# Performance work log

Hardware: AMD Instinct MI355X
Metric: run time of the kernel (lower is better)

Reference implementation:

```python
import jax, jax.numpy as jnp
import numpy as np

B, N, D, H = 4, 4096, 1024, 16
DH = D // H          # per-head dim = 64
M = 256              # number of random features
KEPS = 1e-3          # performer kernel epsilon
LNEPS = 1e-5


def setup_inputs() -> dict:
    key = jax.random.key(0)
    ks = jax.random.split(key, 16)
    s = 0.02
    return {
        "src": jax.random.normal(ks[0], (B, N, D), jnp.float32),
        "Wq": s * jax.random.normal(ks[1], (D, D), jnp.float32),
        "Wk": s * jax.random.normal(ks[2], (D, D), jnp.float32),
        "Wv": s * jax.random.normal(ks[3], (D, D), jnp.float32),
        "Wout": s * jax.random.normal(ks[4], (D, D), jnp.float32),
        "b_out": jnp.zeros((D,), jnp.float32),
        "proj": jax.random.normal(ks[5], (M, DH), jnp.float32),
        "g1": jnp.ones((D,), jnp.float32),
        "beta1": jnp.zeros((D,), jnp.float32),
        "W1": s * jax.random.normal(ks[6], (2048, D), jnp.float32),
        "b1": jnp.zeros((2048,), jnp.float32),
        "W2": s * jax.random.normal(ks[7], (D, 2048), jnp.float32),
        "b2": jnp.zeros((D,), jnp.float32),
        "g2": jnp.ones((D,), jnp.float32),
        "beta2": jnp.zeros((D,), jnp.float32),
    }


def _layernorm(x, g, b):
    mu = x.mean(-1, keepdims=True)
    var = ((x - mu) ** 2).mean(-1, keepdims=True)
    return (x - mu) * jax.lax.rsqrt(var + LNEPS) * g + b


def _softmax_kernel(x, proj, is_query):
    # FAVOR+ positive softmax kernel feature map (performer_pytorch)
    dn = DH ** -0.25           # data normalizer d^{-1/4}
    ratio = M ** -0.5
    data_dash = jnp.einsum('bhnd,md->bhnm', x * dn, proj)
    diag = (x ** 2).sum(-1) * 0.5 * dn * dn            # [b,h,n]
    if is_query:
        stab = data_dash.max(-1, keepdims=True)
    else:
        stab = data_dash.max()
    return ratio * (jnp.exp(data_dash - diag[..., None] - stab) + KEPS)


def reference(src, Wq, Wk, Wv, Wout, b_out, proj, g1, beta1, W1, b1, W2, b2, g2, beta2):
    # ---- Performer self-attention (FAVOR+, non-causal) ----
    def split_heads(x):
        return x.reshape(B, N, H, DH).transpose(0, 2, 1, 3)  # [b,h,n,dh]

    q = split_heads(src @ Wq.T)
    k = split_heads(src @ Wk.T)
    v = split_heads(src @ Wv.T)

    qp = _softmax_kernel(q, proj, is_query=True)   # [b,h,n,m]
    kp = _softmax_kernel(k, proj, is_query=False)  # [b,h,n,m]

    k_sum = kp.sum(-2)                                        # [b,h,m]
    d_inv = 1.0 / jnp.einsum('bhnm,bhm->bhn', qp, k_sum)      # [b,h,n]
    context = jnp.einsum('bhnm,bhnd->bhmd', kp, v)            # [b,h,m,dh]
    attn = jnp.einsum('bhnm,bhmd->bhnd', qp, context) * d_inv[..., None]

    attn = attn.transpose(0, 2, 1, 3).reshape(B, N, D)
    src2 = attn @ Wout.T + b_out

    # ---- residual + norm + FFN (dropout = identity at eval) ----
    x = _layernorm(src + src2, g1, beta1)
    ff = (jax.nn.gelu(x @ W1.T + b1, approximate=False)) @ W2.T + b2
    return _layernorm(x + ff, g2, beta2)
```

## Files before the change

kernel.cpp:

```cpp
#include <hip/hip_runtime.h>

#define DEVI __device__ __forceinline__

using u16 = unsigned short;
using u32 = unsigned int;
using u64 = unsigned long long;

typedef __bf16 bf16x8 __attribute__((ext_vector_type(8)));
typedef __bf16 bf16x4 __attribute__((ext_vector_type(4)));
typedef float  f32x4  __attribute__((ext_vector_type(4)));

constexpr int BB = 4, NN = 4096, DD = 1024, HH = 16, DH = 64, MF = 256;
constexpr int RT = BB * NN;
constexpr int QKVS = 3072;
constexpr float DN    = 0.35355339059327373f;
constexpr float RATIO = 0.0625f;
constexpr float DIAGC = 0.0625f;
constexpr float KEPSC = 1e-3f;

DEVI u16 f2bf(float f) {
  u32 u = __float_as_uint(f);
  u32 r = u + 0x7fffu + ((u >> 16) & 1u);
  return (u16)(r >> 16);
}
DEVI float bf2f(u16 u) { return __uint_as_float(((u32)u) << 16); }

typedef void __attribute__((address_space(1)))* gas1;
typedef void __attribute__((address_space(3)))* las3;
DEVI void gload_lds16(const void* g, void* l) {
  __builtin_amdgcn_global_load_lds((gas1)(u64)g, (las3)(u32)(u64)l, 16, 0, 0);
}

DEVI bf16x8 ldswz(const u16* base, int row, int kbyte) {
  int p = (row << 7) + kbyte;
  p ^= (row & 7) << 4;
  return *(const bf16x8*)((const char*)base + p);
}

__global__ void cast_kernel(const float* __restrict__ in, u16* __restrict__ out, int n4) {
  int i = blockIdx.x * 256 + threadIdx.x;
  int stride = gridDim.x * 256;
  for (; i < n4; i += stride) {
    float4 v = ((const float4*)in)[i];
    ushort4 o; o.x = f2bf(v.x); o.y = f2bf(v.y); o.z = f2bf(v.z); o.w = f2bf(v.w);
    ((ushort4*)out)[i] = o;
  }
}

__global__ void cast_weights_kernel(
    const float* __restrict__ Wq, const float* __restrict__ Wk,
    const float* __restrict__ Wv, const float* __restrict__ Wout,
    const float* __restrict__ W1, const float* __restrict__ W2,
    const float* __restrict__ proj,
    u16* __restrict__ wqkvb, u16* __restrict__ wob,
    u16* __restrict__ w1b, u16* __restrict__ w2b, u16* __restrict__ projb)
{
  constexpr int TOT = 2101248;
  int i = blockIdx.x * 256 + threadIdx.x;
  const int stride = gridDim.x * 256;
  for (; i < TOT; i += stride) {
    const float* s; u16* d; int loc; float sc = 1.0f;
    if (i < 1048576) {
      int seg = i >> 18; loc = i & 262143;
      s = (seg == 0) ? Wq : (seg == 1) ? Wk : (seg == 2) ? Wv : Wout;
      d = (seg < 3) ? (wqkvb + seg * 1048576) : wob;
    } else if (i < 1572864) { loc = i - 1048576; s = W1; d = w1b; }
    else if (i < 2097152)   { loc = i - 1572864; s = W2; d = w2b; }
    else                    { loc = i - 2097152; s = proj; d = projb; sc = DN; }
    float4 v = ((const float4*)s)[loc];
    ushort4 o; o.x = f2bf(v.x * sc); o.y = f2bf(v.y * sc); o.z = f2bf(v.z * sc); o.w = f2bf(v.w * sc);
    ((ushort4*)d)[loc] = o;
  }
}

template <int EPI>
__global__ __launch_bounds__(512, 4) void gemm_bt(
    const u16* __restrict__ A, int lda, const u16* __restrict__ Bm,
    u16* __restrict__ Cb, const float* __restrict__ bias,
    int Ncols, int K)
{
  __shared__ __align__(16) u16 sA[256 * 64];
  __shared__ __align__(16) u16 sB[128 * 64];
  const int tid = threadIdx.x, lane = tid & 63;
  const int wv = tid >> 6, wr = wv >> 1, wc = wv & 1;

  const int gx = gridDim.x;
  const int wg = blockIdx.y * gx + blockIdx.x;
  const int cpx = (gx * gridDim.y) >> 3;
  const int swz = (wg & 7) * cpx + (wg >> 3);
  const int bn = swz % gx, bm = swz / gx;

  f32x4 acc[4][4] = {};

  int rowS[4], colS[4], ldsb[4];
#pragma unroll
  for (int it = 0; it < 4; ++it) {
    int p = (it * 512 + tid) * 16;
    ldsb[it] = (it * 512 + (tid & ~63)) * 16;
    int sp = p ^ (((p >> 7) & 7) << 4);
    rowS[it] = sp >> 7;
    colS[it] = (sp >> 1) & 63;
  }
  const size_t baseA = (size_t)bm * 256, baseB = (size_t)bn * 128;

  for (int kt = 0; kt < K; kt += 64) {
#pragma unroll
    for (int it = 0; it < 4; ++it)
      gload_lds16(A + (baseA + rowS[it]) * lda + kt + colS[it], (char*)sA + ldsb[it]);
#pragma unroll
    for (int it = 0; it < 2; ++it)
      gload_lds16(Bm + (baseB + rowS[it]) * K + kt + colS[it], (char*)sB + ldsb[it]);
    __syncthreads();
#pragma unroll
    for (int kk = 0; kk < 2; ++kk) {
      const int kbyte = kk * 64 + ((lane >> 4) << 4);
      bf16x8 a[4], b[4];
#pragma unroll
      for (int i = 0; i < 4; ++i) a[i] = ldswz(sA, wr * 64 + i * 16 + (lane & 15), kbyte);
#pragma unroll
      for (int i = 0; i < 4; ++i) b[i] = ldswz(sB, wc * 64 + i * 16 + (lane & 15), kbyte);
#pragma unroll
      for (int i = 0; i < 4; ++i)
#pragma unroll
        for (int j = 0; j < 4; ++j)
          acc[i][j] = __builtin_amdgcn_mfma_f32_16x16x32_bf16(a[i], b[j], acc[i][j], 0, 0, 0);
    }
    __syncthreads();
  }

#pragma unroll
  for (int i = 0; i < 4; ++i) {
    const int gr0 = bm * 256 + wr * 64 + i * 16 + ((lane >> 4) << 2);
#pragma unroll
    for (int j = 0; j < 4; ++j) {
      const int gc = bn * 128 + wc * 64 + j * 16 + (lane & 15);
#pragma unroll
      for (int r = 0; r < 4; ++r) {
        const size_t o = (size_t)(gr0 + r) * Ncols + gc;
        const float v = acc[i][j][r];
        if constexpr (EPI == 0) {
          Cb[o] = f2bf(v);
        } else if constexpr (EPI == 2) {
          float t = v + bias[gc];
          Cb[o] = f2bf(0.5f * t * (1.0f + erff(t * 0.70710678118654752f)));
        } else {
          Cb[o] = f2bf(v + bias[gc]);
        }
      }
    }
  }
}

__global__ __launch_bounds__(256) void kmax_kernel(
    const u16* __restrict__ qkvb, const u16* __restrict__ projb, float* __restrict__ pmax)
{
  __shared__ __align__(16) u16 sX[64 * 72];
  __shared__ float sred[4];
  const int tid = threadIdx.x, lane = tid & 63, wv = tid >> 6;
  const int bh = blockIdx.x, b = bh >> 4, h = bh & 15;
  const int n0 = blockIdx.y * 64;

  for (int i = tid; i < 512; i += 256) {
    int r = i >> 3, c8 = (i & 7) << 3;
    uint4 v = *(const uint4*)(qkvb + ((size_t)(b * NN + n0 + r)) * QKVS + 1024 + h * DH + c8);
    *(uint4*)&sX[r * 72 + c8] = v;
  }
  __syncthreads();

  f32x4 dacc[16] = {};
#pragma unroll
  for (int kk = 0; kk < 2; ++kk) {
    const int ko = kk * 32 + ((lane >> 4) << 3);
    bf16x8 a = *(const bf16x8*)&sX[(wv * 16 + (lane & 15)) * 72 + ko];
#pragma unroll
    for (int f = 0; f < 16; ++f) {
      bf16x8 bb = *(const bf16x8*)(projb + (f * 16 + (lane & 15)) * 64 + ko);
      dacc[f] = __builtin_amdgcn_mfma_f32_16x16x32_bf16(a, bb, dacc[f], 0, 0, 0);
    }
  }
  float mx = -1e30f;
#pragma unroll
  for (int f = 0; f < 16; ++f)
#pragma unroll
    for (int r = 0; r < 4; ++r) mx = fmaxf(mx, dacc[f][r]);
#pragma unroll
  for (int m = 1; m < 64; m <<= 1) mx = fmaxf(mx, __shfl_xor(mx, m));
  if (lane == 0) sred[wv] = mx;
  __syncthreads();
  if (tid == 0)
    pmax[blockIdx.y * gridDim.x + blockIdx.x] =
        fmaxf(fmaxf(sred[0], sred[1]), fmaxf(sred[2], sred[3]));
}

__global__ __launch_bounds__(256) void reduce_max_kernel(
    const float* __restrict__ pmax, float* __restrict__ stab)
{
  const int tid = threadIdx.x;
  float mx = -1e30f;
#pragma unroll
  for (int i = 0; i < 16; ++i) mx = fmaxf(mx, pmax[i * 256 + tid]);
#pragma unroll
  for (int m = 1; m < 64; m <<= 1) mx = fmaxf(mx, __shfl_xor(mx, m));
  __shared__ float sred[4];
  if ((tid & 63) == 0) sred[tid >> 6] = mx;
  __syncthreads();
  if (tid == 0)
    stab[0] = fmaxf(fmaxf(sred[0], sred[1]), fmaxf(sred[2], sred[3]));
}

__global__ __launch_bounds__(256, 4) void kctx_kernel(
    const u16* __restrict__ qkvb, const u16* __restrict__ projb,
    const float* __restrict__ stab_p,
    float* __restrict__ ctxT, float* __restrict__ ksum)
{
  __shared__ __align__(16) u16 sX[64 * 72];
  __shared__ __align__(16) u16 sVT[64 * 68];
  __shared__ __align__(16) u16 sKpT[128 * 72];
  __shared__ float sDiag[64];
  const int tid = threadIdx.x, lane = tid & 63, wv = tid >> 6;
  const int bh = blockIdx.x, b = bh >> 4, h = bh & 15;
  const int sl = blockIdx.y >> 1, mh = blockIdx.y & 1;
  const float stab = stab_p[0];

  f32x4 cacc[8] = {};
  float ksacc[8] = {};
  const int row_base = wv * 16 + ((lane >> 4) << 2);

  for (int t = 0; t < 8; ++t) {
    const int n0 = sl * 512 + t * 64;
    if (t) __syncthreads();
#pragma unroll
    for (int it = 0; it < 2; ++it) {
      int i = it * 256 + tid;
      int r = i >> 3, c8 = (i & 7) << 3;
      size_t g = ((size_t)(b * NN + n0 + r)) * QKVS + h * DH + c8;
      uint4 xv = *(const uint4*)(qkvb + g + 1024);
      *(uint4*)&sX[r * 72 + c8] = xv;
      {
        const u16* px = (const u16*)&xv;
        float s = 0;
#pragma unroll
        for (int j = 0; j < 8; ++j) { float x = bf2f(px[j]); s += x * x; }
        s += __shfl_xor(s, 1); s += __shfl_xor(s, 2); s += __shfl_xor(s, 4);
        if ((tid & 7) == 0) sDiag[r] = DIAGC * s;
      }
      uint4 vv = *(const uint4*)(qkvb + g + 2048);
      const u16* pv = (const u16*)&vv;
#pragma unroll
      for (int j = 0; j < 8; ++j) sVT[(c8 + j) * 68 + r] = pv[j];
    }
    __syncthreads();

    f32x4 dacc[8] = {};
#pragma unroll
    for (int kk = 0; kk < 2; ++kk) {
      const int ko = kk * 32 + ((lane >> 4) << 3);
      bf16x8 a = *(const bf16x8*)&sX[(wv * 16 + (lane & 15)) * 72 + ko];
#pragma unroll
      for (int f = 0; f < 8; ++f) {
        bf16x8 bb = *(const bf16x8*)(projb + (mh * 128 + f * 16 + (lane & 15)) * 64 + ko);
        dacc[f] = __builtin_amdgcn_mfma_f32_16x16x32_bf16(a, bb, dacc[f], 0, 0, 0);
      }
    }
#pragma unroll
    for (int f = 0; f < 8; ++f) {
      float kvv[4]; float cs = 0;
#pragma unroll
      for (int r = 0; r < 4; ++r) {
        float val = RATIO * (__expf(dacc[f][r] - sDiag[row_base + r] - stab) + KEPSC);
        kvv[r] = val; cs += val;
      }
      cs += __shfl_xor(cs, 16); cs += __shfl_xor(cs, 32);
      ksacc[f] += cs;
      ushort4 pk; pk.x = f2bf(kvv[0]); pk.y = f2bf(kvv[1]); pk.z = f2bf(kvv[2]); pk.w = f2bf(kvv[3]);
      *(ushort4*)&sKpT[(f * 16 + (lane & 15)) * 72 + row_base] = pk;
    }
    __syncthreads();
#pragma unroll
    for (int kk = 0; kk < 2; ++kk) {
      const int ko = kk * 32 + ((lane >> 4) << 3);
      const int vrow = wv * 16 + (lane & 15);
      bf16x4 lo = *(const bf16x4*)&sVT[vrow * 68 + ko];
      bf16x4 hi = *(const bf16x4*)&sVT[vrow * 68 + ko + 4];
      bf16x8 a;
#pragma unroll
      for (int e = 0; e < 4; ++e) { a[e] = lo[e]; a[e + 4] = hi[e]; }
#pragma unroll
      for (int f = 0; f < 8; ++f) {
        bf16x8 bb = *(const bf16x8*)&sKpT[(f * 16 + (lane & 15)) * 72 + ko];
        cacc[f] = __builtin_amdgcn_mfma_f32_16x16x32_bf16(a, bb, cacc[f], 0, 0, 0);
      }
    }
  }
#pragma unroll
  for (int f = 0; f < 8; ++f) {
    const int m = mh * 128 + f * 16 + (lane & 15);
#pragma unroll
    for (int r = 0; r < 4; ++r)
      atomicAdd(&ctxT[((size_t)bh * 64 + row_base + r) * 256 + m], cacc[f][r]);
  }
  if (lane < 16) {
#pragma unroll
    for (int f = 0; f < 8; ++f)
      atomicAdd(&ksum[bh * 256 + mh * 128 + f * 16 + lane], ksacc[f]);
  }
}

__global__ __launch_bounds__(256) void ctxfin_kernel(
    const float* __restrict__ ctxT, u16* __restrict__ ctxb)
{
  const int i = blockIdx.x * 256 + threadIdx.x;
  float4 v = ((const float4*)ctxT)[i];
  ushort4 o; o.x = f2bf(v.x); o.y = f2bf(v.y); o.z = f2bf(v.z); o.w = f2bf(v.w);
  ((ushort4*)ctxb)[i] = o;
}

__global__ __launch_bounds__(256, 2) void qattn_kernel(
    u16* qkvb, const u16* __restrict__ projb,
    const u16* __restrict__ ctxb, const float* __restrict__ ksum)
{
  __shared__ __align__(16) u16 sCtx[64 * 256];
  __shared__ __align__(16) u16 sX[64 * 72];
  __shared__ __align__(16) u16 sQp[64 * 264];
  __shared__ float sKsum[256];
  __shared__ float sDiag[64];
  __shared__ float sDinv[64];
  const int tid = threadIdx.x, lane = tid & 63, wv = tid >> 6;
  const int bh = blockIdx.x, b = bh >> 4, h = bh & 15;

  {
    const char* cbase = (const char*)(ctxb + (size_t)bh * 16384);
#pragma unroll
    for (int it = 0; it < 8; ++it) {
      int p = (it * 256 + tid) * 16;
      int ldsb = (it * 256 + (tid & ~63)) * 16;
      int q = p ^ (((p >> 9) & 7) << 4);
      gload_lds16(cbase + q, (char*)sCtx + ldsb);
    }
  }
  sKsum[tid] = ksum[bh * 256 + tid];

  const int row_base = wv * 16 + ((lane >> 4) << 2);
  const int wr = wv >> 1, wc = wv & 1;

  for (int rt = 0; rt < 2; ++rt) {
    const int n0 = (blockIdx.y * 2 + rt) * 64;
    for (int i = tid; i < 512; i += 256) {
      int r = i >> 3, c8 = (i & 7) << 3;
      uint4 v = *(const uint4*)(qkvb + ((size_t)(b * NN + n0 + r)) * QKVS + h * DH + c8);
      *(uint4*)&sX[r * 72 + c8] = v;
    }
    __syncthreads();
    {
      int r = tid >> 2, qq = tid & 3;
      float s = 0;
#pragma unroll
      for (int j = 0; j < 16; ++j) { float x = bf2f(sX[r * 72 + qq * 16 + j]); s += x * x; }
      s += __shfl_xor(s, 1); s += __shfl_xor(s, 2);
      if (qq == 0) sDiag[r] = DIAGC * s;
    }
    f32x4 dacc[16] = {};
#pragma unroll
    for (int kk = 0; kk < 2; ++kk) {
      const int ko = kk * 32 + ((lane >> 4) << 3);
      bf16x8 a = *(const bf16x8*)&sX[(wv * 16 + (lane & 15)) * 72 + ko];
#pragma unroll
      for (int f = 0; f < 16; ++f) {
        bf16x8 bb = *(const bf16x8*)(projb + (f * 16 + (lane & 15)) * 64 + ko);
        dacc[f] = __builtin_amdgcn_mfma_f32_16x16x32_bf16(a, bb, dacc[f], 0, 0, 0);
      }
    }
    __syncthreads();
#pragma unroll
    for (int r = 0; r < 4; ++r) {
      const int row = row_base + r;
      float mx = dacc[0][r];
#pragma unroll
      for (int f = 1; f < 16; ++f) mx = fmaxf(mx, dacc[f][r]);
      mx = fmaxf(mx, __shfl_xor(mx, 1));
      mx = fmaxf(mx, __shfl_xor(mx, 2));
      mx = fmaxf(mx, __shfl_xor(mx, 4));
      mx = fmaxf(mx, __shfl_xor(mx, 8));
      const float dg = sDiag[row];
      float ds = 0;
#pragma unroll
      for (int f = 0; f < 16; ++f) {
        float qv = RATIO * (__expf(dacc[f][r] - dg - mx) + KEPSC);
        dacc[f][r] = qv;
        ds += qv * sKsum[f * 16 + (lane & 15)];
      }
      ds += __shfl_xor(ds, 1); ds += __shfl_xor(ds, 2);
      ds += __shfl_xor(ds, 4); ds += __shfl_xor(ds, 8);
      if ((lane & 15) == 0) sDinv[row] = 1.0f / ds;
    }
#pragma unroll
    for (int f = 0; f < 16; ++f)
#pragma unroll
      for (int r = 0; r < 4; ++r)
        sQp[(row_base + r) * 264 + f * 16 + (lane & 15)] = f2bf(dacc[f][r]);
    __syncthreads();

    f32x4 acc2[2][2] = {};
#pragma unroll
    for (int kk = 0; kk < 8; ++kk) {
      const int koe = kk * 32 + ((lane >> 4) << 3);
      const int kob = koe * 2;
      bf16x8 a0 = *(const bf16x8*)&sQp[(wr * 32 + (lane & 15)) * 264 + koe];
      bf16x8 a1 = *(const bf16x8*)&sQp[(wr * 32 + 16 + (lane & 15)) * 264 + koe];
      const int j0 = wc * 32 + (lane & 15), j1 = j0 + 16;
      bf16x8 b0 = *(const bf16x8*)((const char*)sCtx + (((j0 << 9) + kob) ^ ((j0 & 7) << 4)));
      bf16x8 b1 = *(const bf16x8*)((const char*)sCtx + (((j1 << 9) + kob) ^ ((j1 & 7) << 4)));
      acc2[0][0] = __builtin_amdgcn_mfma_f32_16x16x32_bf16(a0, b0, acc2[0][0], 0, 0, 0);
      acc2[0][1] = __builtin_amdgcn_mfma_f32_16x16x32_bf16(a0, b1, acc2[0][1], 0, 0, 0);
      acc2[1][0] = __builtin_amdgcn_mfma_f32_16x16x32_bf16(a1, b0, acc2[1][0], 0, 0, 0);
      acc2[1][1] = __builtin_amdgcn_mfma_f32_16x16x32_bf16(a1, b1, acc2[1][1], 0, 0, 0);
    }
#pragma unroll
    for (int mi = 0; mi < 2; ++mi)
#pragma unroll
      for (int ni = 0; ni < 2; ++ni)
#pragma unroll
        for (int r = 0; r < 4; ++r) {
          const int row = wr * 32 + mi * 16 + ((lane >> 4) << 2) + r;
          const int col = wc * 32 + ni * 16 + (lane & 15);
          float v = acc2[mi][ni][r] * sDinv[row];
          qkvb[((size_t)(b * NN + n0 + row)) * QKVS + h * DH + col] = f2bf(v);
        }
    __syncthreads();
  }
}

__global__ __launch_bounds__(256) void ln1_kernel(
    const float* __restrict__ src, const u16* __restrict__ wout,
    const float* __restrict__ g, const float* __restrict__ be, u16* __restrict__ xb)
{
  const int row = blockIdx.x, tid = threadIdx.x;
  const float4 sv = ((const float4*)(src + (size_t)row * DD))[tid];
  const ushort4 wv = ((const ushort4*)(wout + (size_t)row * DD))[tid];
  float x0 = sv.x + bf2f(wv.x);
  float x1 = sv.y + bf2f(wv.y);
  float x2 = sv.z + bf2f(wv.z);
  float x3 = sv.w + bf2f(wv.w);
  float s = x0 + x1 + x2 + x3;
  float ss = x0 * x0 + x1 * x1 + x2 * x2 + x3 * x3;
#pragma unroll
  for (int m = 1; m < 64; m <<= 1) { s += __shfl_xor(s, m); ss += __shfl_xor(ss, m); }
  __shared__ float red[8];
  if ((tid & 63) == 0) { red[tid >> 6] = s; red[4 + (tid >> 6)] = ss; }
  __syncthreads();
  s = red[0] + red[1] + red[2] + red[3];
  ss = red[4] + red[5] + red[6] + red[7];
  const float mu = s * (1.0f / DD);
  const float rs = rsqrtf(ss * (1.0f / DD) - mu * mu + 1e-5f);
  const float4 gv = ((const float4*)g)[tid];
  const float4 bv = ((const float4*)be)[tid];
  ushort4 o;
  o.x = f2bf((x0 - mu) * rs * gv.x + bv.x);
  o.y = f2bf((x1 - mu) * rs * gv.y + bv.y);
  o.z = f2bf((x2 - mu) * rs * gv.z + bv.z);
  o.w = f2bf((x3 - mu) * rs * gv.w + bv.w);
  ((ushort4*)(xb + (size_t)row * DD))[tid] = o;
}

__global__ __launch_bounds__(256) void ln2_kernel(
    const u16* __restrict__ xb, const u16* __restrict__ ff,
    const float* __restrict__ g, const float* __restrict__ be, float* __restrict__ out)
{
  const int row = blockIdx.x, tid = threadIdx.x;
  const ushort4 xv = ((const ushort4*)(xb + (size_t)row * DD))[tid];
  const ushort4 fv = ((const ushort4*)(ff + (size_t)row * DD))[tid];
  float x0 = bf2f(xv.x) + bf2f(fv.x);
  float x1 = bf2f(xv.y) + bf2f(fv.y);
  float x2 = bf2f(xv.z) + bf2f(fv.z);
  float x3 = bf2f(xv.w) + bf2f(fv.w);
  float s = x0 + x1 + x2 + x3;
  float ss = x0 * x0 + x1 * x1 + x2 * x2 + x3 * x3;
#pragma unroll
  for (int m = 1; m < 64; m <<= 1) { s += __shfl_xor(s, m); ss += __shfl_xor(ss, m); }
  __shared__ float red[8];
  if ((tid & 63) == 0) { red[tid >> 6] = s; red[4 + (tid >> 6)] = ss; }
  __syncthreads();
  s = red[0] + red[1] + red[2] + red[3];
  ss = red[4] + red[5] + red[6] + red[7];
  const float mu = s * (1.0f / DD);
  const float rs = rsqrtf(ss * (1.0f / DD) - mu * mu + 1e-5f);
  const float4 gv = ((const float4*)g)[tid];
  const float4 bv = ((const float4*)be)[tid];
  float4 o;
  o.x = (x0 - mu) * rs * gv.x + bv.x;
  o.y = (x1 - mu) * rs * gv.y + bv.y;
  o.z = (x2 - mu) * rs * gv.z + bv.z;
  o.w = (x3 - mu) * rs * gv.w + bv.w;
  ((float4*)(out + (size_t)row * DD))[tid] = o;
}

extern "C" void kernel_launch(void* const* d_in, const int* in_sizes, int n_in,
                              void* d_out, int out_size, void* d_ws, size_t ws_size,
                              hipStream_t stream) {
  (void)in_sizes; (void)n_in; (void)out_size; (void)ws_size;
  const float* src   = (const float*)d_in[0];
  const float* Wq    = (const float*)d_in[1];
  const float* Wk    = (const float*)d_in[2];
  const float* Wv    = (const float*)d_in[3];
  const float* Wout  = (const float*)d_in[4];
  const float* b_out = (const float*)d_in[5];
  const float* proj  = (const float*)d_in[6];
  const float* g1    = (const float*)d_in[7];
  const float* be1   = (const float*)d_in[8];
  const float* W1    = (const float*)d_in[9];
  const float* b1    = (const float*)d_in[10];
  const float* W2    = (const float*)d_in[11];
  const float* b2    = (const float*)d_in[12];
  const float* g2    = (const float*)d_in[13];
  const float* be2   = (const float*)d_in[14];

  char* ws = (char*)d_ws;
  constexpr size_t OFF_SRCB = 0;
  constexpr size_t OFF_QKV  = 33554432;
  constexpr size_t OFF_XB   = 67108864;
  constexpr size_t OFF_WOUTB= 100663296;
  constexpr size_t OFF_WQKV = 134217728;
  constexpr size_t OFF_WO   = 140509184;
  constexpr size_t OFF_W1   = 142606336;
  constexpr size_t OFF_W2   = 146800640;
  constexpr size_t OFF_PROJ = 150994944;
  constexpr size_t OFF_CTXT = 151027712;
  constexpr size_t OFF_KSUM = 155222016;
  constexpr size_t OFF_PMAX = 155287552;
  constexpr size_t OFF_STAB = 155303936;

  u16* srcb  = (u16*)(ws + OFF_SRCB);
  u16* qkvb  = (u16*)(ws + OFF_QKV);
  u16* wqkvb = (u16*)(ws + OFF_WQKV);
  u16* wob   = (u16*)(ws + OFF_WO);
  u16* w1b   = (u16*)(ws + OFF_W1);
  u16* w2b   = (u16*)(ws + OFF_W2);
  u16* projb = (u16*)(ws + OFF_PROJ);
  float* ctxT = (float*)(ws + OFF_CTXT);
  float* ksum = (float*)(ws + OFF_KSUM);
  float* pmax = (float*)(ws + OFF_PMAX);
  float* stab = (float*)(ws + OFF_STAB);
  u16* ctxb  = (u16*)(ws + OFF_SRCB);
  u16* woutb = (u16*)(ws + OFF_WOUTB);
  u16* xb    = (u16*)(ws + OFF_XB);
  u16* h1    = (u16*)(ws + OFF_SRCB);
  u16* ff    = (u16*)(ws + OFF_WOUTB);

  cast_kernel<<<4096, 256, 0, stream>>>(src, srcb, RT * DD / 4);
  cast_weights_kernel<<<2048, 256, 0, stream>>>(Wq, Wk, Wv, Wout, W1, W2, proj,
                                                wqkvb, wob, w1b, w2b, projb);
  hipMemsetAsync(ws + OFF_CTXT, 0, 4194304 + 65536, stream);

  gemm_bt<0><<<dim3(QKVS / 128, RT / 256), 512, 0, stream>>>(srcb, DD, wqkvb, qkvb, nullptr, QKVS, DD);

  kmax_kernel<<<dim3(64, 64), 256, 0, stream>>>(qkvb, projb, pmax);
  reduce_max_kernel<<<1, 256, 0, stream>>>(pmax, stab);
  kctx_kernel<<<dim3(64, 16), 256, 0, stream>>>(qkvb, projb, stab, ctxT, ksum);
  ctxfin_kernel<<<4096, 256, 0, stream>>>(ctxT, ctxb);
  qattn_kernel<<<dim3(64, 32), 256, 0, stream>>>(qkvb, projb, ctxb, ksum);

  gemm_bt<3><<<dim3(DD / 128, RT / 256), 512, 0, stream>>>(qkvb, QKVS, wob, woutb, b_out, DD, DD);
  ln1_kernel<<<RT, 256, 0, stream>>>(src, woutb, g1, be1, xb);

  gemm_bt<2><<<dim3(2048 / 128, RT / 256), 512, 0, stream>>>(xb, DD, w1b, h1, b1, 2048, DD);
  gemm_bt<3><<<dim3(DD / 128, RT / 256), 512, 0, stream>>>(h1, 2048, w2b, ff, b2, DD, 2048);
  ln2_kernel<<<RT, 256, 0, stream>>>(xb, ff, g2, be2, (float*)d_out);
}
```

Before: 739.2 us.

## Shrink GEMM tiles to 128x128 and replace kctx atomics with per-slice partial buffers

The GEMM kernel moves from 256x128 tiles with 512 threads to 128x128 tiles with 256 threads. This doubles the grid, trading operand reuse per block for more blocks in flight. The kctx kernel now computes both feature halves in one 512-thread block that shares the staged K/V tiles. Each sequence slice writes its context partials to a separate buffer instead of using float atomics, and ctxfin sums the 8 partials. This drops the atomic traffic and most of the memset, but adds a larger fp32 partial buffer that has to be read back.

```diff
diff --git a/kernel.cpp b/kernel.cpp
--- a/kernel.cpp
+++ b/kernel.cpp
@@ -74,12 +74,12 @@
 }
 
 template <int EPI>
-__global__ __launch_bounds__(512, 4) void gemm_bt(
+__global__ __launch_bounds__(256, 2) void gemm_bt(
     const u16* __restrict__ A, int lda, const u16* __restrict__ Bm,
     u16* __restrict__ Cb, const float* __restrict__ bias,
     int Ncols, int K)
 {
-  __shared__ __align__(16) u16 sA[256 * 64];
+  __shared__ __align__(16) u16 sA[128 * 64];
   __shared__ __align__(16) u16 sB[128 * 64];
   const int tid = threadIdx.x, lane = tid & 63;
   const int wv = tid >> 6, wr = wv >> 1, wc = wv & 1;
@@ -95,20 +95,20 @@
   int rowS[4], colS[4], ldsb[4];
 #pragma unroll
   for (int it = 0; it < 4; ++it) {
-    int p = (it * 512 + tid) * 16;
-    ldsb[it] = (it * 512 + (tid & ~63)) * 16;
+    int p = (it * 256 + tid) * 16;
+    ldsb[it] = (it * 256 + (tid & ~63)) * 16;
     int sp = p ^ (((p >> 7) & 7) << 4);
     rowS[it] = sp >> 7;
     colS[it] = (sp >> 1) & 63;
   }
-  const size_t baseA = (size_t)bm * 256, baseB = (size_t)bn * 128;
+  const size_t baseA = (size_t)bm * 128, baseB = (size_t)bn * 128;
 
   for (int kt = 0; kt < K; kt += 64) {
 #pragma unroll
     for (int it = 0; it < 4; ++it)
       gload_lds16(A + (baseA + rowS[it]) * lda + kt + colS[it], (char*)sA + ldsb[it]);
 #pragma unroll
-    for (int it = 0; it < 2; ++it)
+    for (int it = 0; it < 4; ++it)
       gload_lds16(Bm + (baseB + rowS[it]) * K + kt + colS[it], (char*)sB + ldsb[it]);
     __syncthreads();
 #pragma unroll
@@ -130,7 +130,7 @@
 
 #pragma unroll
   for (int i = 0; i < 4; ++i) {
-    const int gr0 = bm * 256 + wr * 64 + i * 16 + ((lane >> 4) << 2);
+    const int gr0 = bm * 128 + wr * 64 + i * 16 + ((lane >> 4) << 2);
 #pragma unroll
     for (int j = 0; j < 4; ++j) {
       const int gc = bn * 128 + wc * 64 + j * 16 + (lane & 15);
@@ -208,31 +208,31 @@
     stab[0] = fmaxf(fmaxf(sred[0], sred[1]), fmaxf(sred[2], sred[3]));
 }
 
-__global__ __launch_bounds__(256, 4) void kctx_kernel(
+__global__ __launch_bounds__(512, 4) void kctx_kernel(
     const u16* __restrict__ qkvb, const u16* __restrict__ projb,
     const float* __restrict__ stab_p,
-    float* __restrict__ ctxT, float* __restrict__ ksum)
+    float* __restrict__ ctxP, float* __restrict__ ksum)
 {
   __shared__ __align__(16) u16 sX[64 * 72];
   __shared__ __align__(16) u16 sVT[64 * 68];
-  __shared__ __align__(16) u16 sKpT[128 * 72];
+  __shared__ __align__(16) u16 sKpT[256 * 72];
   __shared__ float sDiag[64];
   const int tid = threadIdx.x, lane = tid & 63, wv = tid >> 6;
+  const int nw = wv & 3;
+  const int mh = wv >> 2;
   const int bh = blockIdx.x, b = bh >> 4, h = bh & 15;
-  const int sl = blockIdx.y >> 1, mh = blockIdx.y & 1;
+  const int sl = blockIdx.y;
   const float stab = stab_p[0];
 
   f32x4 cacc[8] = {};
   float ksacc[8] = {};
-  const int row_base = wv * 16 + ((lane >> 4) << 2);
+  const int row_base = nw * 16 + ((lane >> 4) << 2);
 
   for (int t = 0; t < 8; ++t) {
     const int n0 = sl * 512 + t * 64;
     if (t) __syncthreads();
-#pragma unroll
-    for (int it = 0; it < 2; ++it) {
-      int i = it * 256 + tid;
-      int r = i >> 3, c8 = (i & 7) << 3;
+    {
+      int r = tid >> 3, c8 = (tid & 7) << 3;
       size_t g = ((size_t)(b * NN + n0 + r)) * QKVS + h * DH + c8;
       uint4 xv = *(const uint4*)(qkvb + g + 1024);
       *(uint4*)&sX[r * 72 + c8] = xv;
@@ -255,7 +255,7 @@
 #pragma unroll
     for (int kk = 0; kk < 2; ++kk) {
       const int ko = kk * 32 + ((lane >> 4) << 3);
-      bf16x8 a = *(const bf16x8*)&sX[(wv * 16 + (lane & 15)) * 72 + ko];
+      bf16x8 a = *(const bf16x8*)&sX[(nw * 16 + (lane & 15)) * 72 + ko];
 #pragma unroll
       for (int f = 0; f < 8; ++f) {
         bf16x8 bb = *(const bf16x8*)(projb + (mh * 128 + f * 16 + (lane & 15)) * 64 + ko);
@@ -273,13 +273,13 @@
       cs += __shfl_xor(cs, 16); cs += __shfl_xor(cs, 32);
       ksacc[f] += cs;
       ushort4 pk; pk.x = f2bf(kvv[0]); pk.y = f2bf(kvv[1]); pk.z = f2bf(kvv[2]); pk.w = f2bf(kvv[3]);
-      *(ushort4*)&sKpT[(f * 16 + (lane & 15)) * 72 + row_base] = pk;
+      *(ushort4*)&sKpT[(mh * 128 + f * 16 + (lane & 15)) * 72 + row_base] = pk;
     }
     __syncthreads();
 #pragma unroll
     for (int kk = 0; kk < 2; ++kk) {
       const int ko = kk * 32 + ((lane >> 4) << 3);
-      const int vrow = wv * 16 + (lane & 15);
+      const int vrow = nw * 16 + (lane & 15);
       bf16x4 lo = *(const bf16x4*)&sVT[vrow * 68 + ko];
       bf16x4 hi = *(const bf16x4*)&sVT[vrow * 68 + ko + 4];
       bf16x8 a;
@@ -287,17 +287,18 @@
       for (int e = 0; e < 4; ++e) { a[e] = lo[e]; a[e + 4] = hi[e]; }
 #pragma unroll
       for (int f = 0; f < 8; ++f) {
-        bf16x8 bb = *(const bf16x8*)&sKpT[(f * 16 + (lane & 15)) * 72 + ko];
+        bf16x8 bb = *(const bf16x8*)&sKpT[(mh * 128 + f * 16 + (lane & 15)) * 72 + ko];
         cacc[f] = __builtin_amdgcn_mfma_f32_16x16x32_bf16(a, bb, cacc[f], 0, 0, 0);
       }
     }
   }
+  float* cp = ctxP + (size_t)(sl * 64 + bh) * 16384;
 #pragma unroll
   for (int f = 0; f < 8; ++f) {
     const int m = mh * 128 + f * 16 + (lane & 15);
 #pragma unroll
     for (int r = 0; r < 4; ++r)
-      atomicAdd(&ctxT[((size_t)bh * 64 + row_base + r) * 256 + m], cacc[f][r]);
+      cp[(row_base + r) * 256 + m] = cacc[f][r];
   }
   if (lane < 16) {
 #pragma unroll
@@ -307,12 +308,18 @@
 }
 
 __global__ __launch_bounds__(256) void ctxfin_kernel(
-    const float* __restrict__ ctxT, u16* __restrict__ ctxb)
-{
-  const int i = blockIdx.x * 256 + threadIdx.x;
-  float4 v = ((const float4*)ctxT)[i];
-  ushort4 o; o.x = f2bf(v.x); o.y = f2bf(v.y); o.z = f2bf(v.z); o.w = f2bf(v.w);
-  ((ushort4*)ctxb)[i] = o;
+    const float* __restrict__ ctxP, u16* __restrict__ ctxb)
+{
+  const int idx = blockIdx.x * 256 + threadIdx.x;
+  const int bh = idx >> 12, pos = idx & 4095;
+  float4 s = {0, 0, 0, 0};
+#pragma unroll
+  for (int sl = 0; sl < 8; ++sl) {
+    float4 v = *(const float4*)(ctxP + (size_t)(sl * 64 + bh) * 16384 + pos * 4);
+    s.x += v.x; s.y += v.y; s.z += v.z; s.w += v.w;
+  }
+  ushort4 o; o.x = f2bf(s.x); o.y = f2bf(s.y); o.z = f2bf(s.z); o.w = f2bf(s.w);
+  *(ushort4*)(ctxb + (size_t)bh * 16384 + pos * 4) = o;
 }
 
 __global__ __launch_bounds__(256, 2) void qattn_kernel(
@@ -524,10 +531,10 @@
   constexpr size_t OFF_W1   = 142606336;
   constexpr size_t OFF_W2   = 146800640;
   constexpr size_t OFF_PROJ = 150994944;
-  constexpr size_t OFF_CTXT = 151027712;
-  constexpr size_t OFF_KSUM = 155222016;
-  constexpr size_t OFF_PMAX = 155287552;
-  constexpr size_t OFF_STAB = 155303936;
+  constexpr size_t OFF_CTXB = 151027712;
+  constexpr size_t OFF_KSUM = 153124864;
+  constexpr size_t OFF_PMAX = 153190400;
+  constexpr size_t OFF_STAB = 153206784;
 
   u16* srcb  = (u16*)(ws + OFF_SRCB);
   u16* qkvb  = (u16*)(ws + OFF_QKV);
@@ -536,11 +543,11 @@
   u16* w1b   = (u16*)(ws + OFF_W1);
   u16* w2b   = (u16*)(ws + OFF_W2);
   u16* projb = (u16*)(ws + OFF_PROJ);
-  float* ctxT = (float*)(ws + OFF_CTXT);
+  u16* ctxb  = (u16*)(ws + OFF_CTXB);
   float* ksum = (float*)(ws + OFF_KSUM);
   float* pmax = (float*)(ws + OFF_PMAX);
   float* stab = (float*)(ws + OFF_STAB);
-  u16* ctxb  = (u16*)(ws + OFF_SRCB);
+  float* ctxP = (float*)(ws + OFF_SRCB);
   u16* woutb = (u16*)(ws + OFF_WOUTB);
   u16* xb    = (u16*)(ws + OFF_XB);
   u16* h1    = (u16*)(ws + OFF_SRCB);
@@ -549,20 +556,20 @@
   cast_kernel<<<4096, 256, 0, stream>>>(src, srcb, RT * DD / 4);
   cast_weights_kernel<<<2048, 256, 0, stream>>>(Wq, Wk, Wv, Wout, W1, W2, proj,
                                                 wqkvb, wob, w1b, w2b, projb);
-  hipMemsetAsync(ws + OFF_CTXT, 0, 4194304 + 65536, stream);
-
-  gemm_bt<0><<<dim3(QKVS / 128, RT / 256), 512, 0, stream>>>(srcb, DD, wqkvb, qkvb, nullptr, QKVS, DD);
+  hipMemsetAsync(ws + OFF_KSUM, 0, 65536, stream);
+
+  gemm_bt<0><<<dim3(QKVS / 128, RT / 128), 256, 0, stream>>>(srcb, DD, wqkvb, qkvb, nullptr, QKVS, DD);
 
   kmax_kernel<<<dim3(64, 64), 256, 0, stream>>>(qkvb, projb, pmax);
   reduce_max_kernel<<<1, 256, 0, stream>>>(pmax, stab);
-  kctx_kernel<<<dim3(64, 16), 256, 0, stream>>>(qkvb, projb, stab, ctxT, ksum);
-  ctxfin_kernel<<<4096, 256, 0, stream>>>(ctxT, ctxb);
+  kctx_kernel<<<dim3(64, 8), 512, 0, stream>>>(qkvb, projb, stab, ctxP, ksum);
+  ctxfin_kernel<<<1024, 256, 0, stream>>>(ctxP, ctxb);
   qattn_kernel<<<dim3(64, 32), 256, 0, stream>>>(qkvb, projb, ctxb, ksum);
 
-  gemm_bt<3><<<dim3(DD / 128, RT / 256), 512, 0, stream>>>(qkvb, QKVS, wob, woutb, b_out, DD, DD);
+  gemm_bt<3><<<dim3(DD / 128, RT / 128), 256, 0, stream>>>(qkvb, QKVS, wob, woutb, b_out, DD, DD);
   ln1_kernel<<<RT, 256, 0, stream>>>(src, woutb, g1, be1, xb);
 
-  gemm_bt<2><<<dim3(2048 / 128, RT / 256), 512, 0, stream>>>(xb, DD, w1b, h1, b1, 2048, DD);
-  gemm_bt<3><<<dim3(DD / 128, RT / 256), 512, 0, stream>>>(h1, 2048, w2b, ff, b2, DD, 2048);
+  gemm_bt<2><<<dim3(2048 / 128, RT / 128), 256, 0, stream>>>(xb, DD, w1b, h1, b1, 2048, DD);
+  gemm_bt<3><<<dim3(DD / 128, RT / 128), 256, 0, stream>>>(h1, 2048, w2b, ff, b2, DD, 2048);
   ln2_kernel<<<RT, 256, 0, stream>>>(xb, ff, g2, be2, (float*)d_out);
 }
```

New measurement: 779.1 us. 5.4% more time.
